# Kernel tuning notes

Measured on AMD Instinct MI355X. Metric: run time of the kernel, lower is better.

Reference implementation:

```python
import jax, jax.numpy as jnp
import numpy as np

B, T, A, F_IN = 32, 128, 22, 32
H1, C1 = 4, 128  # heads, gnn_hidden_dim
NEG_SLOPE = 0.2  # GATConv default leaky_relu slope


def setup_inputs() -> dict:
    key = jax.random.key(0)
    ks = jax.random.split(key, 12)
    g = lambda k, shape: jax.random.normal(k, shape, dtype=jnp.float32) * 0.05
    d1 = H1 * C1  # 512, concat output dim of multi-head layers
    return {
        "features": jax.random.normal(ks[0], (B, T, A, F_IN), dtype=jnp.float32),
        "W1": g(ks[1], (F_IN, H1, C1)), "as1": g(ks[2], (H1, C1)), "ad1": g(ks[3], (H1, C1)), "b1": jnp.zeros((d1,), jnp.float32),
        "W2": g(ks[4], (d1, H1, C1)), "as2": g(ks[5], (H1, C1)), "ad2": g(ks[6], (H1, C1)), "b2": jnp.zeros((d1,), jnp.float32),
        "W3": g(ks[7], (d1, 1, C1)), "as3": g(ks[8], (1, C1)), "ad3": g(ks[9], (1, C1)), "b3": jnp.zeros((C1,), jnp.float32),
        "Wc": g(ks[10], (C1, 1)), "bc": jnp.zeros((1,), jnp.float32),
    }


def _gat(x, W, a_src, a_dst, b, concat):
    # x: [G, A, F]; complete graph + self loops == dense attention over all A nodes.
    h = jnp.einsum('gaf,fhc->gahc', x, W)           # [G, A, H, C]
    s = jnp.einsum('gahc,hc->gha', h, a_src)        # att_src . h_j
    d = jnp.einsum('gahc,hc->gha', h, a_dst)        # att_dst . h_i
    logits = d[:, :, :, None] + s[:, :, None, :]    # [G, H, i, j] edge j->i
    logits = jnp.where(logits >= 0, logits, NEG_SLOPE * logits)
    alpha = jax.nn.softmax(logits, axis=-1)         # softmax over source nodes j
    out = jnp.einsum('ghij,gjhc->gihc', alpha, h)   # [G, A, H, C]
    G_, A_, H_, C_ = out.shape
    out = out.reshape(G_, A_, H_ * C_) if concat else out.mean(axis=2)
    return out + b


def reference(features, W1, as1, ad1, b1, W2, as2, ad2, b2, W3, as3, ad3, b3, Wc, bc):
    Bb, Tt, Aa, Ff = features.shape
    x = features.reshape(Bb * Tt, Aa, Ff)           # [G, A, F], G = B*T frame-graphs
    x = jax.nn.relu(_gat(x, W1, as1, ad1, b1, True))
    x = jax.nn.relu(_gat(x, W2, as2, ad2, b2, True))
    x = jax.nn.relu(_gat(x, W3, as3, ad3, b3, False))
    pooled = x.mean(axis=1)                         # global_mean_pool over 22 agents
    return (pooled @ Wc + bc)[:, 0]                 # [G] logits
```

## Files before the change

### kernel.cpp

```cpp
#include <hip/hip_runtime.h>

typedef unsigned short u16;
typedef unsigned int   u32;
typedef unsigned long long u64;
typedef short bf16x8 __attribute__((ext_vector_type(8)));
typedef float f32x4  __attribute__((ext_vector_type(4)));

#define NA 22
#define FIN 32
#define XS_STR 520
#define AL_STR 24

#define W1_OFF 0
#define W2_OFF 16384
#define W3_OFF 278528
#define E1_OFF 344064
#define E2_OFF 344576
#define E3_OFF 352768
#define WS_TOTAL 360960

__device__ float b2f(u16 u) {
    return __uint_as_float(((unsigned int)u) << 16);
}

__device__ u16 f2b(float f) {
    unsigned int x = __float_as_uint(f);
    x = (x + 0x7fffu + ((x >> 16) & 1u)) >> 16;
    return (u16)x;
}

__device__ __forceinline__ u32 pack2(float a, float b) {
    return (u32)f2b(a) | ((u32)f2b(b) << 16);
}

__global__ void swizzle_kernel(const float* W1, const float* W2, const float* W3, u16* ws)
{
    int t = blockIdx.x * 256 + threadIdx.x;
    const float* W; int NT, nshift, base, loc;
    if (t < W2_OFF)      { W = W1; NT = 32; nshift = 9; base = W1_OFF; loc = t; }
    else if (t < W3_OFF) { W = W2; NT = 32; nshift = 9; base = W2_OFF; loc = t - W2_OFF; }
    else if (t < E1_OFF) { W = W3; NT = 8;  nshift = 7; base = W3_OFF; loc = t - W3_OFF; }
    else { return; }
    int k = loc >> nshift;
    int n = loc & ((1 << nshift) - 1);
    u16 v = f2b(W[loc]);
    int kt = k >> 5, quad = (k & 31) >> 3, j = k & 7;
    int nt = n >> 4, lm = n & 15;
    int lane = (quad << 4) | lm;
    ws[base + (((kt * NT + nt) << 9) | (lane << 3) | j)] = v;
}

__global__ void wav_kernel(const float* W1, const float* as1, const float* ad1,
                           const float* W2, const float* as2, const float* ad2,
                           const float* W3, const float* as3, const float* ad3,
                           u16* ws)
{
    int t = blockIdx.x * 256 + threadIdx.x;
    const float* W; const float* asp; const float* adp;
    int H, N, base, loc;
    if (t < 512)        { W = W1; asp = as1; adp = ad1; H = 4; N = 512; base = E1_OFF; loc = t; }
    else if (t < 8704)  { W = W2; asp = as2; adp = ad2; H = 4; N = 512; base = E2_OFF; loc = t - 512; }
    else if (t < 16896) { W = W3; asp = as3; adp = ad3; H = 1; N = 128; base = E3_OFF; loc = t - 8704; }
    else { return; }
    int kt = loc >> 9, r = loc & 511;
    int lane = r >> 3, j = r & 7;
    int quad = lane >> 4, lm = lane & 15;
    u16 outv = 0;
    if (lm < 2 * H) {
        int h = (H == 4) ? (lm & 3) : 0;
        int which = (H == 4) ? (lm >> 2) : lm;
        const float* av = which ? adp : asp;
        int k = kt * 32 + quad * 8 + j;
        float s = 0.f;
        for (int c = 0; c < 128; ++c) { s += W[k * N + h * 128 + c] * av[h * 128 + c]; }
        outv = f2b(s);
    }
    ws[base + (kt << 9) + (lane << 3) + j] = outv;
}

template<int KT, int NT, int NTW, int H>
__device__ __forceinline__ void gat_layer(
    const u16* Wsw, const u16* Wext, const float* bias,
    u16* xs, float* svw, u16* al)
{
    int tid  = threadIdx.x;
    int wave = tid >> 6, lane = tid & 63;
    int quad = lane >> 4, lm = lane & 15;
    int r1 = 16 + lm; if (r1 >= NA) { r1 = lm; }

    f32x4 acc0[NTW], acc1[NTW], accE0, accE1;

    {
        const u16* a0base = xs + lm * XS_STR + quad * 8;
        const u16* a1base = xs + r1 * XS_STR + quad * 8;
        const u16* wbase  = Wsw + ((wave * NTW) << 9) + (lane << 3);
        const u16* ebase  = Wext + (lane << 3);

        f32x4 z4 = {0.f, 0.f, 0.f, 0.f};
        #pragma unroll
        for (int n = 0; n < NTW; ++n) { acc0[n] = z4; acc1[n] = z4; }
        accE0 = z4; accE1 = z4;

        bf16x8 bbuf[2][NTW], ebuf[2], ab0[2], ab1[2];
        #pragma unroll
        for (int n = 0; n < NTW; ++n) { bbuf[0][n] = *(const bf16x8*)(wbase + (n << 9)); }
        ebuf[0] = *(const bf16x8*)(ebase);
        ab0[0] = *(const bf16x8*)(a0base);
        ab1[0] = *(const bf16x8*)(a1base);

        #pragma unroll
        for (int kt = 0; kt < KT; ++kt) {
            const int cur = kt & 1;
            const int nxt = cur ^ 1;
            if (kt + 1 < KT) {
                const u16* wn = wbase + (((kt + 1) * NT) << 9);
                #pragma unroll
                for (int n = 0; n < NTW; ++n) { bbuf[nxt][n] = *(const bf16x8*)(wn + (n << 9)); }
                ebuf[nxt] = *(const bf16x8*)(ebase + ((kt + 1) << 9));
                ab0[nxt] = *(const bf16x8*)(a0base + (kt + 1) * 32);
                ab1[nxt] = *(const bf16x8*)(a1base + (kt + 1) * 32);
            }
            #pragma unroll
            for (int n = 0; n < NTW; ++n) {
                acc0[n] = __builtin_amdgcn_mfma_f32_16x16x32_bf16(ab0[cur], bbuf[cur][n], acc0[n], 0, 0, 0);
                acc1[n] = __builtin_amdgcn_mfma_f32_16x16x32_bf16(ab1[cur], bbuf[cur][n], acc1[n], 0, 0, 0);
            }
            accE0 = __builtin_amdgcn_mfma_f32_16x16x32_bf16(ab0[cur], ebuf[cur], accE0, 0, 0, 0);
            accE1 = __builtin_amdgcn_mfma_f32_16x16x32_bf16(ab1[cur], ebuf[cur], accE1, 0, 0, 0);
        }
    }

    int head = (H == 4) ? (wave >> 1) : 0;
    float* sw = svw + wave * 48;
    if (lm == head) {
        #pragma unroll
        for (int r = 0; r < 4; ++r) {
            sw[quad * 4 + r] = accE0[r];
            int row1 = 16 + quad * 4 + r;
            if (row1 < NA) { sw[row1] = accE1[r]; }
        }
    }
    if (lm == head + H) {
        #pragma unroll
        for (int r = 0; r < 4; ++r) {
            sw[24 + quad * 4 + r] = accE0[r];
            int row1 = 16 + quad * 4 + r;
            if (row1 < NA) { sw[24 + row1] = accE1[r]; }
        }
    }

    bf16x8 bfrag[NTW];
    {
        int s0 = (((quad & 1) << 5) | lm) << 2;
        int s2 = s0 + 64;
        bool hi = (quad >= 2);
        #pragma unroll
        for (int n = 0; n < NTW; ++n) {
            u32 P0a = pack2(acc0[n][0], acc0[n][1]);
            u32 P1a = pack2(acc0[n][2], acc0[n][3]);
            u32 P0b = pack2(acc1[n][0], acc1[n][1]);
            u32 P1b = pack2(acc1[n][2], acc1[n][3]);
            u32 w0a = (u32)__builtin_amdgcn_ds_bpermute(s0, (int)P0a);
            u32 w0b = (u32)__builtin_amdgcn_ds_bpermute(s0, (int)P0b);
            u32 w1a = (u32)__builtin_amdgcn_ds_bpermute(s0, (int)P1a);
            u32 w1b = (u32)__builtin_amdgcn_ds_bpermute(s0, (int)P1b);
            u32 w2a = (u32)__builtin_amdgcn_ds_bpermute(s2, (int)P0a);
            u32 w2b = (u32)__builtin_amdgcn_ds_bpermute(s2, (int)P0b);
            u32 w3a = (u32)__builtin_amdgcn_ds_bpermute(s2, (int)P1a);
            u32 w3b = (u32)__builtin_amdgcn_ds_bpermute(s2, (int)P1b);
            union { u32 w[4]; bf16x8 v; } bu;
            bu.w[0] = hi ? w0b : w0a;
            bu.w[1] = hi ? w1b : w1a;
            bu.w[2] = hi ? w2b : w2a;
            bu.w[3] = hi ? w3b : w3a;
            bfrag[n] = bu.v;
        }
    }

    if (lane < NA) {
        float di = sw[24 + lane];
        float lg[NA];
        float mx = -1.0e30f, ss = 0.0f;
        #pragma unroll
        for (int j = 0; j < NA; ++j) {
            float l = di + sw[j];
            l = fmaxf(l, 0.2f * l);
            lg[j] = l;
            mx = fmaxf(mx, l);
        }
        #pragma unroll
        for (int j = 0; j < NA; ++j) {
            float e = __expf(lg[j] - mx);
            lg[j] = e;
            ss += e;
        }
        float inv = 1.0f / ss;
        u16* arow = al + (wave * NA + lane) * AL_STR;
        #pragma unroll
        for (int j = 0; j < NA; ++j) { arow[j] = f2b(lg[j] * inv); }
        arow[22] = 0; arow[23] = 0;
    }

    const u16* albase = al + wave * NA * AL_STR;
    bf16x8 zb = {0, 0, 0, 0, 0, 0, 0, 0};
    bf16x8 pa0 = (quad < 3) ? *(const bf16x8*)(albase + lm * AL_STR + quad * 8) : zb;
    bf16x8 pa1 = (quad < 3) ? *(const bf16x8*)(albase + r1 * AL_STR + quad * 8) : zb;

    f32x4 agg0[NTW], agg1[NTW];
    f32x4 z4 = {0.f, 0.f, 0.f, 0.f};
    float bv[NTW];
    #pragma unroll
    for (int n = 0; n < NTW; ++n) {
        int col = (wave * NTW + n) * 16 + lm;
        bv[n] = bias[col];
        agg0[n] = __builtin_amdgcn_mfma_f32_16x16x32_bf16(pa0, bfrag[n], z4, 0, 0, 0);
        agg1[n] = __builtin_amdgcn_mfma_f32_16x16x32_bf16(pa1, bfrag[n], z4, 0, 0, 0);
    }

    __syncthreads();

    #pragma unroll
    for (int n = 0; n < NTW; ++n) {
        int col = (wave * NTW + n) * 16 + lm;
        #pragma unroll
        for (int r = 0; r < 4; ++r) {
            int row0 = quad * 4 + r;
            xs[row0 * XS_STR + col] = f2b(fmaxf(agg0[n][r] + bv[n], 0.0f));
            int row1 = 16 + quad * 4 + r;
            if (row1 < NA) {
                xs[row1 * XS_STR + col] = f2b(fmaxf(agg1[n][r] + bv[n], 0.0f));
            }
        }
    }
    __syncthreads();
}

__global__ void __launch_bounds__(512, 3)
pressgnn_kernel(const float* feats, const u16* ws,
                const float* b1, const float* b2, const float* b3,
                const float* Wc, const float* bc,
                float* out)
{
    __shared__ __align__(16) u16 xs[NA * XS_STR];
    __shared__ __align__(16) u16 al[8 * NA * AL_STR];
    __shared__ __align__(16) float svw[8 * 48];
    __shared__ float pool[128];

    int g = blockIdx.x;
    int tid = threadIdx.x;

    for (int i = tid; i < NA * FIN; i += 512) {
        int row = i >> 5;
        int col = i & 31;
        xs[row * XS_STR + col] = f2b(feats[g * NA * FIN + i]);
    }
    __syncthreads();

    gat_layer<1,  32, 4, 4>(ws + W1_OFF, ws + E1_OFF, b1, xs, svw, al);
    gat_layer<16, 32, 4, 4>(ws + W2_OFF, ws + E2_OFF, b2, xs, svw, al);
    gat_layer<16, 8,  1, 1>(ws + W3_OFF, ws + E3_OFF, b3, xs, svw, al);

    if (tid < 128) {
        float s = 0.0f;
        #pragma unroll
        for (int a = 0; a < NA; ++a) { s += b2f(xs[a * XS_STR + tid]); }
        pool[tid] = (s / 22.0f) * Wc[tid];
    }
    __syncthreads();
    if (tid < 64) {
        float s = pool[tid] + pool[tid + 64];
        #pragma unroll
        for (int off = 32; off > 0; off >>= 1) { s += __shfl_down(s, off); }
        if (tid == 0) { out[g] = s + bc[0]; }
    }
}

extern "C" void kernel_launch(void* const* d_in, const int* in_sizes, int n_in,
                              void* d_out, int out_size, void* d_ws, size_t ws_size,
                              hipStream_t stream) {
    const float* feats = (const float*)d_in[0];
    const float* W1  = (const float*)d_in[1];
    const float* as1 = (const float*)d_in[2];
    const float* ad1 = (const float*)d_in[3];
    const float* b1  = (const float*)d_in[4];
    const float* W2  = (const float*)d_in[5];
    const float* as2 = (const float*)d_in[6];
    const float* ad2 = (const float*)d_in[7];
    const float* b2  = (const float*)d_in[8];
    const float* W3  = (const float*)d_in[9];
    const float* as3 = (const float*)d_in[10];
    const float* ad3 = (const float*)d_in[11];
    const float* b3  = (const float*)d_in[12];
    const float* Wc  = (const float*)d_in[13];
    const float* bc  = (const float*)d_in[14];
    float* out = (float*)d_out;
    u16* ws = (u16*)d_ws;

    swizzle_kernel<<<dim3(1344), dim3(256), 0, stream>>>(W1, W2, W3, ws);
    wav_kernel<<<dim3(66), dim3(256), 0, stream>>>(W1, as1, ad1, W2, as2, ad2,
                                                   W3, as3, ad3, ws);

    pressgnn_kernel<<<dim3(out_size), dim3(512), 0, stream>>>(
        feats, ws, b1, b2, b3, Wc, bc, out);
}
```

Baseline: 263.2 us.

## Fuse final GAT layer with mean-pool and classifier, use hardware bf16 pack

Replaces software bf16 rounding with the v_cvt_pk_bf16_f32 instruction. Alpha rows are written as vectorized 16-byte stores, and one bpermute per tile is dropped because those lanes only carry padding rows. A specialized final layer reduces the third GAT output straight into the pooled classifier result using shuffles, so the last xs writeback, a barrier and the LDS pooling pass go away. The layer writeback also skips rows past the 22 agents. This cuts ALU and LDS traffic at the cost of more specialized code and relies on the inline asm existing on the target.

New measurement: 254.1 us. 3.5% less time.

```diff
diff --git a/kernel.cpp b/kernel.cpp
--- a/kernel.cpp
+++ b/kernel.cpp
@@ -5,6 +5,7 @@
 typedef unsigned long long u64;
 typedef short bf16x8 __attribute__((ext_vector_type(8)));
 typedef float f32x4  __attribute__((ext_vector_type(4)));
+typedef u32   u32x4  __attribute__((ext_vector_type(4)));
 
 #define NA 22
 #define FIN 32
@@ -29,8 +30,10 @@
     return (u16)x;
 }
 
-__device__ __forceinline__ u32 pack2(float a, float b) {
-    return (u32)f2b(a) | ((u32)f2b(b) << 16);
+__device__ __forceinline__ u32 cvtpk(float lo, float hi) {
+    u32 r;
+    asm("v_cvt_pk_bf16_f32 %0, %1, %2" : "=v"(r) : "v"(lo), "v"(hi));
+    return r;
 }
 
 __global__ void swizzle_kernel(const float* W1, const float* W2, const float* W3, u16* ws)
@@ -78,6 +81,7 @@
     ws[base + (kt << 9) + (lane << 3) + j] = outv;
 }
 
+
 template<int KT, int NT, int NTW, int H>
 __device__ __forceinline__ void gat_layer(
     const u16* Wsw, const u16* Wext, const float* bias,
@@ -156,10 +160,10 @@
         bool hi = (quad >= 2);
         #pragma unroll
         for (int n = 0; n < NTW; ++n) {
-            u32 P0a = pack2(acc0[n][0], acc0[n][1]);
-            u32 P1a = pack2(acc0[n][2], acc0[n][3]);
-            u32 P0b = pack2(acc1[n][0], acc1[n][1]);
-            u32 P1b = pack2(acc1[n][2], acc1[n][3]);
+            u32 P0a = cvtpk(acc0[n][0], acc0[n][1]);
+            u32 P1a = cvtpk(acc0[n][2], acc0[n][3]);
+            u32 P0b = cvtpk(acc1[n][0], acc1[n][1]);
+            u32 P1b = cvtpk(acc1[n][2], acc1[n][3]);
             u32 w0a = (u32)__builtin_amdgcn_ds_bpermute(s0, (int)P0a);
             u32 w0b = (u32)__builtin_amdgcn_ds_bpermute(s0, (int)P0b);
             u32 w1a = (u32)__builtin_amdgcn_ds_bpermute(s0, (int)P1a);
@@ -167,12 +171,11 @@
             u32 w2a = (u32)__builtin_amdgcn_ds_bpermute(s2, (int)P0a);
             u32 w2b = (u32)__builtin_amdgcn_ds_bpermute(s2, (int)P0b);
             u32 w3a = (u32)__builtin_amdgcn_ds_bpermute(s2, (int)P1a);
-            u32 w3b = (u32)__builtin_amdgcn_ds_bpermute(s2, (int)P1b);
             union { u32 w[4]; bf16x8 v; } bu;
             bu.w[0] = hi ? w0b : w0a;
             bu.w[1] = hi ? w1b : w1a;
             bu.w[2] = hi ? w2b : w2a;
-            bu.w[3] = hi ? w3b : w3a;
+            bu.w[3] = hi ? 0u  : w3a;
             bfrag[n] = bu.v;
         }
     }
@@ -195,10 +198,19 @@
             ss += e;
         }
         float inv = 1.0f / ss;
-        u16* arow = al + (wave * NA + lane) * AL_STR;
-        #pragma unroll
-        for (int j = 0; j < NA; ++j) { arow[j] = f2b(lg[j] * inv); }
-        arow[22] = 0; arow[23] = 0;
+        u32 pk[12];
+        #pragma unroll
+        for (int j2 = 0; j2 < 11; ++j2) {
+            pk[j2] = cvtpk(lg[2 * j2] * inv, lg[2 * j2 + 1] * inv);
+        }
+        pk[11] = 0;
+        u32* arow = (u32*)(al + (wave * NA + lane) * AL_STR);
+        u32x4 q0 = {pk[0], pk[1], pk[2],  pk[3]};
+        u32x4 q1 = {pk[4], pk[5], pk[6],  pk[7]};
+        u32x4 q2 = {pk[8], pk[9], pk[10], pk[11]};
+        *(u32x4*)(arow)     = q0;
+        *(u32x4*)(arow + 4) = q1;
+        *(u32x4*)(arow + 8) = q2;
     }
 
     const u16* albase = al + wave * NA * AL_STR;
@@ -222,17 +234,190 @@
     #pragma unroll
     for (int n = 0; n < NTW; ++n) {
         int col = (wave * NTW + n) * 16 + lm;
+        u16* cbase = xs + col;
+        float v0 = fmaxf(agg0[n][0] + bv[n], 0.0f);
+        float v1 = fmaxf(agg0[n][1] + bv[n], 0.0f);
+        float v2 = fmaxf(agg0[n][2] + bv[n], 0.0f);
+        float v3 = fmaxf(agg0[n][3] + bv[n], 0.0f);
+        u32 wa0 = cvtpk(v0, v1), wa1 = cvtpk(v2, v3);
+        int r0 = quad * 4;
+        cbase[(r0 + 0) * XS_STR] = (u16)wa0;
+        cbase[(r0 + 1) * XS_STR] = (u16)(wa0 >> 16);
+        cbase[(r0 + 2) * XS_STR] = (u16)wa1;
+        cbase[(r0 + 3) * XS_STR] = (u16)(wa1 >> 16);
+        if (quad < 2) {
+            float u0 = fmaxf(agg1[n][0] + bv[n], 0.0f);
+            float u1 = fmaxf(agg1[n][1] + bv[n], 0.0f);
+            u32 wb0 = cvtpk(u0, u1);
+            int r16 = 16 + quad * 4;
+            cbase[(r16 + 0) * XS_STR] = (u16)wb0;
+            cbase[(r16 + 1) * XS_STR] = (u16)(wb0 >> 16);
+            if (quad == 0) {
+                float u2 = fmaxf(agg1[n][2] + bv[n], 0.0f);
+                float u3 = fmaxf(agg1[n][3] + bv[n], 0.0f);
+                u32 wb1 = cvtpk(u2, u3);
+                cbase[18 * XS_STR] = (u16)wb1;
+                cbase[19 * XS_STR] = (u16)(wb1 >> 16);
+            }
+        }
+    }
+    __syncthreads();
+}
+
+template<int KT, int NT>
+__device__ __forceinline__ void gat_final(
+    const u16* Wsw, const u16* Wext, const float* bias,
+    const u16* xs, float* svw, u16* al,
+    const float* Wc, const float* bc, float* partial, float* out, int g)
+{
+    int tid  = threadIdx.x;
+    int wave = tid >> 6, lane = tid & 63;
+    int quad = lane >> 4, lm = lane & 15;
+    int r1 = 16 + lm; if (r1 >= NA) { r1 = lm; }
+
+    f32x4 acc0, acc1, accE0, accE1;
+
+    {
+        const u16* a0base = xs + lm * XS_STR + quad * 8;
+        const u16* a1base = xs + r1 * XS_STR + quad * 8;
+        const u16* wbase  = Wsw + (wave << 9) + (lane << 3);
+        const u16* ebase  = Wext + (lane << 3);
+
+        f32x4 z4 = {0.f, 0.f, 0.f, 0.f};
+        acc0 = z4; acc1 = z4; accE0 = z4; accE1 = z4;
+
+        bf16x8 bbuf[2], ebuf[2], ab0[2], ab1[2];
+        bbuf[0] = *(const bf16x8*)(wbase);
+        ebuf[0] = *(const bf16x8*)(ebase);
+        ab0[0] = *(const bf16x8*)(a0base);
+        ab1[0] = *(const bf16x8*)(a1base);
+
+        #pragma unroll
+        for (int kt = 0; kt < KT; ++kt) {
+            const int cur = kt & 1;
+            const int nxt = cur ^ 1;
+            if (kt + 1 < KT) {
+                bbuf[nxt] = *(const bf16x8*)(wbase + (((kt + 1) * NT) << 9));
+                ebuf[nxt] = *(const bf16x8*)(ebase + ((kt + 1) << 9));
+                ab0[nxt] = *(const bf16x8*)(a0base + (kt + 1) * 32);
+                ab1[nxt] = *(const bf16x8*)(a1base + (kt + 1) * 32);
+            }
+            acc0  = __builtin_amdgcn_mfma_f32_16x16x32_bf16(ab0[cur], bbuf[cur], acc0, 0, 0, 0);
+            acc1  = __builtin_amdgcn_mfma_f32_16x16x32_bf16(ab1[cur], bbuf[cur], acc1, 0, 0, 0);
+            accE0 = __builtin_amdgcn_mfma_f32_16x16x32_bf16(ab0[cur], ebuf[cur], accE0, 0, 0, 0);
+            accE1 = __builtin_amdgcn_mfma_f32_16x16x32_bf16(ab1[cur], ebuf[cur], accE1, 0, 0, 0);
+        }
+    }
+
+    float* sw = svw + wave * 48;
+    if (lm == 0) {
         #pragma unroll
         for (int r = 0; r < 4; ++r) {
-            int row0 = quad * 4 + r;
-            xs[row0 * XS_STR + col] = f2b(fmaxf(agg0[n][r] + bv[n], 0.0f));
+            sw[quad * 4 + r] = accE0[r];
             int row1 = 16 + quad * 4 + r;
-            if (row1 < NA) {
-                xs[row1 * XS_STR + col] = f2b(fmaxf(agg1[n][r] + bv[n], 0.0f));
-            }
-        }
-    }
+            if (row1 < NA) { sw[row1] = accE1[r]; }
+        }
+    }
+    if (lm == 1) {
+        #pragma unroll
+        for (int r = 0; r < 4; ++r) {
+            sw[24 + quad * 4 + r] = accE0[r];
+            int row1 = 16 + quad * 4 + r;
+            if (row1 < NA) { sw[24 + row1] = accE1[r]; }
+        }
+    }
+
+    bf16x8 bfrag;
+    {
+        int s0 = (((quad & 1) << 5) | lm) << 2;
+        int s2 = s0 + 64;
+        bool hi = (quad >= 2);
+        u32 P0a = cvtpk(acc0[0], acc0[1]);
+        u32 P1a = cvtpk(acc0[2], acc0[3]);
+        u32 P0b = cvtpk(acc1[0], acc1[1]);
+        u32 P1b = cvtpk(acc1[2], acc1[3]);
+        u32 w0a = (u32)__builtin_amdgcn_ds_bpermute(s0, (int)P0a);
+        u32 w0b = (u32)__builtin_amdgcn_ds_bpermute(s0, (int)P0b);
+        u32 w1a = (u32)__builtin_amdgcn_ds_bpermute(s0, (int)P1a);
+        u32 w1b = (u32)__builtin_amdgcn_ds_bpermute(s0, (int)P1b);
+        u32 w2a = (u32)__builtin_amdgcn_ds_bpermute(s2, (int)P0a);
+        u32 w2b = (u32)__builtin_amdgcn_ds_bpermute(s2, (int)P0b);
+        u32 w3a = (u32)__builtin_amdgcn_ds_bpermute(s2, (int)P1a);
+        union { u32 w[4]; bf16x8 v; } bu;
+        bu.w[0] = hi ? w0b : w0a;
+        bu.w[1] = hi ? w1b : w1a;
+        bu.w[2] = hi ? w2b : w2a;
+        bu.w[3] = hi ? 0u  : w3a;
+        bfrag = bu.v;
+    }
+
+    if (lane < NA) {
+        float di = sw[24 + lane];
+        float lg[NA];
+        float mx = -1.0e30f, ss = 0.0f;
+        #pragma unroll
+        for (int j = 0; j < NA; ++j) {
+            float l = di + sw[j];
+            l = fmaxf(l, 0.2f * l);
+            lg[j] = l;
+            mx = fmaxf(mx, l);
+        }
+        #pragma unroll
+        for (int j = 0; j < NA; ++j) {
+            float e = __expf(lg[j] - mx);
+            lg[j] = e;
+            ss += e;
+        }
+        float inv = 1.0f / ss;
+        u32 pk[12];
+        #pragma unroll
+        for (int j2 = 0; j2 < 11; ++j2) {
+            pk[j2] = cvtpk(lg[2 * j2] * inv, lg[2 * j2 + 1] * inv);
+        }
+        pk[11] = 0;
+        u32* arow = (u32*)(al + (wave * NA + lane) * AL_STR);
+        u32x4 q0 = {pk[0], pk[1], pk[2],  pk[3]};
+        u32x4 q1 = {pk[4], pk[5], pk[6],  pk[7]};
+        u32x4 q2 = {pk[8], pk[9], pk[10], pk[11]};
+        *(u32x4*)(arow)     = q0;
+        *(u32x4*)(arow + 4) = q1;
+        *(u32x4*)(arow + 8) = q2;
+    }
+
+    const u16* albase = al + wave * NA * AL_STR;
+    bf16x8 zb = {0, 0, 0, 0, 0, 0, 0, 0};
+    bf16x8 pa0 = (quad < 3) ? *(const bf16x8*)(albase + lm * AL_STR + quad * 8) : zb;
+    bf16x8 pa1 = (quad < 3) ? *(const bf16x8*)(albase + r1 * AL_STR + quad * 8) : zb;
+
+    f32x4 z4 = {0.f, 0.f, 0.f, 0.f};
+    f32x4 agg0 = __builtin_amdgcn_mfma_f32_16x16x32_bf16(pa0, bfrag, z4, 0, 0, 0);
+    f32x4 agg1 = __builtin_amdgcn_mfma_f32_16x16x32_bf16(pa1, bfrag, z4, 0, 0, 0);
+
+    int col = wave * 16 + lm;
+    float bvv = bias[col];
+    float cs = 0.0f;
+    #pragma unroll
+    for (int r = 0; r < 4; ++r) { cs += fmaxf(agg0[r] + bvv, 0.0f); }
+    #pragma unroll
+    for (int r = 0; r < 4; ++r) {
+        int row1 = 16 + quad * 4 + r;
+        if (row1 < NA) { cs += fmaxf(agg1[r] + bvv, 0.0f); }
+    }
+    cs += __shfl_xor(cs, 16);
+    cs += __shfl_xor(cs, 32);
+    float part = (cs / 22.0f) * Wc[col];
+    part += __shfl_xor(part, 1);
+    part += __shfl_xor(part, 2);
+    part += __shfl_xor(part, 4);
+    part += __shfl_xor(part, 8);
+    if (lane == 0) { partial[wave] = part; }
     __syncthreads();
+    if (tid == 0) {
+        float t = 0.0f;
+        #pragma unroll
+        for (int w = 0; w < 8; ++w) { t += partial[w]; }
+        out[g] = t + bc[0];
+    }
 }
 
 __global__ void __launch_bounds__(512, 3)
@@ -244,7 +429,7 @@
     __shared__ __align__(16) u16 xs[NA * XS_STR];
     __shared__ __align__(16) u16 al[8 * NA * AL_STR];
     __shared__ __align__(16) float svw[8 * 48];
-    __shared__ float pool[128];
+    __shared__ float partial[8];
 
     int g = blockIdx.x;
     int tid = threadIdx.x;
@@ -258,21 +443,8 @@
 
     gat_layer<1,  32, 4, 4>(ws + W1_OFF, ws + E1_OFF, b1, xs, svw, al);
     gat_layer<16, 32, 4, 4>(ws + W2_OFF, ws + E2_OFF, b2, xs, svw, al);
-    gat_layer<16, 8,  1, 1>(ws + W3_OFF, ws + E3_OFF, b3, xs, svw, al);
-
-    if (tid < 128) {
-        float s = 0.0f;
-        #pragma unroll
-        for (int a = 0; a < NA; ++a) { s += b2f(xs[a * XS_STR + tid]); }
-        pool[tid] = (s / 22.0f) * Wc[tid];
-    }
-    __syncthreads();
-    if (tid < 64) {
-        float s = pool[tid] + pool[tid + 64];
-        #pragma unroll
-        for (int off = 32; off > 0; off >>= 1) { s += __shfl_down(s, off); }
-        if (tid == 0) { out[g] = s + bc[0]; }
-    }
+    gat_final<16, 8>(ws + W3_OFF, ws + E3_OFF, b3, xs, svw, al,
+                     Wc, bc, partial, out, g);
 }
 
 extern "C" void kernel_launch(void* const* d_in, const int* in_sizes, int n_in,
```
